# Kernel optimization log

Hardware: AMD Instinct MI355X
Metric: run time of the kernel (lower is better)

Reference implementation:

```python
import jax, jax.numpy as jnp
import numpy as np
import math

B, CZ, L = 1, 128, 256
H, C = 4, 32  # num_heads, head dim
EPS = 1e-5


def _conv1x1(w, x):
    # w: (out, in), x: (b, in, i, j) -> (b, out, i, j)
    return jnp.einsum('oc,bcij->boij', w, x)


def setup_inputs() -> dict:
    key = jax.random.key(0)
    ks = jax.random.split(key, 8)
    s = 1.0 / math.sqrt(CZ)
    return {
        'pair_rep': jax.random.normal(ks[0], (B, CZ, L, L), jnp.float32),
        'ln_gamma': jnp.ones((CZ, L, L), jnp.float32),
        'ln_beta': jnp.zeros((CZ, L, L), jnp.float32),
        'w_q': jax.random.normal(ks[1], (H * C, CZ), jnp.float32) * s,
        'w_k': jax.random.normal(ks[2], (H * C, CZ), jnp.float32) * s,
        'w_v': jax.random.normal(ks[3], (H * C, CZ), jnp.float32) * s,
        'w_b': jax.random.normal(ks[4], (H, CZ), jnp.float32) * s,
        'w_g': jax.random.normal(ks[5], (H * C, CZ), jnp.float32) * s,
        'b_g': jnp.zeros((H * C,), jnp.float32),
        'w_rep': jax.random.normal(ks[6], (CZ, H * C), jnp.float32) * s,
        'b_rep': jnp.zeros((CZ,), jnp.float32),
    }


def reference(pair_rep, ln_gamma, ln_beta, w_q, w_k, w_v, w_b, w_g, b_g, w_rep, b_rep):
    # LayerNorm over (c_z, h, w) jointly, full-shape affine (torch LayerNorm([c_z,h,w]))
    mu = jnp.mean(pair_rep, axis=(1, 2, 3), keepdims=True)
    var = jnp.var(pair_rep, axis=(1, 2, 3), keepdims=True)
    x = (pair_rep - mu) * jax.lax.rsqrt(var + EPS) * ln_gamma[None] + ln_beta[None]

    # 1x1 conv projections; channels packed as (h c): channel = h*C + c
    q = _conv1x1(w_q, x).reshape(B, H, C, L, L)  # bhcij
    k = _conv1x1(w_k, x).reshape(B, H, C, L, L)
    v = _conv1x1(w_v, x).reshape(B, H, C, L, L)
    bias = _conv1x1(w_b, x)                       # (b, h, i, j) -> used as bias[b,h,j,k]
    g = jax.nn.sigmoid(_conv1x1(w_g, x) + b_g[None, :, None, None]).reshape(B, H, C, L, L)

    scale = 1.0 / math.sqrt(C)
    # scores[b,h,i,j,k] = scale * sum_c q[b,h,c,i,j] k[b,h,c,i,k] + bias[b,h,j,k]
    scores = scale * jnp.einsum('bhcij,bhcik->bhijk', q, k) + bias[:, :, None, :, :]
    a = jax.nn.softmax(scores, axis=-1)
    # o[b,h,c,i,j] = sum_k a[b,h,i,j,k] v[b,h,c,i,k]  (same math as the 6D broadcast-sum)
    o = g * jnp.einsum('bhijk,bhcik->bhcij', a, v)

    # output repacks channels as (c h): channel = c*H + h
    o = jnp.transpose(o, (0, 2, 1, 3, 4)).reshape(B, C * H, L, L)
    return _conv1x1(w_rep, o) + b_rep[None, :, None, None]
```

## Files before the change

kernel.cpp:

```cpp
#include <hip/hip_runtime.h>
#include <math.h>

#define L 256
#define CZ 128
#define NH 4
#define HD 32
#define P (L*L)
#define NTOT (CZ*P)
#define EPSV 1e-5f
#define SCALE 0.17677669529663687f

typedef unsigned short u16;
typedef _Float16 f16;
typedef __attribute__((ext_vector_type(8))) _Float16 f16x8;
typedef __attribute__((ext_vector_type(4))) _Float16 f16x4;
typedef __attribute__((ext_vector_type(4))) float    f32x4;

__device__ __forceinline__ float bu2f(u16 u){ return __uint_as_float(((unsigned)u) << 16); }
__device__ __forceinline__ u16 f2bu(float x){
  unsigned u = __float_as_uint(x);
  return (u16)((u + 0x7fffu + ((u >> 16) & 1u)) >> 16);
}

__device__ __forceinline__ float ldr(bool fp32, const void* p, size_t i){
  return fp32 ? ((const float*)p)[i] : bu2f(((const u16*)p)[i]);
}
__device__ __forceinline__ void str(bool fp32, void* p, size_t i, float v){
  if (fp32) ((float*)p)[i] = v; else ((u16*)p)[i] = f2bu(v);
}
template<bool FP32>
__device__ __forceinline__ float ldin(const void* p, size_t i){
  return FP32 ? ((const float*)p)[i] : bu2f(((const u16*)p)[i]);
}
template<bool FP32>
__device__ __forceinline__ void stout(void* p, size_t i, float v){
  if (FP32) ((float*)p)[i] = v; else ((u16*)p)[i] = f2bu(v);
}

__device__ __forceinline__ void glds16(const void* g, void* l){
  __builtin_amdgcn_global_load_lds((const __attribute__((address_space(1))) void*)g,
                                   (__attribute__((address_space(3))) void*)l, 16, 0, 0);
}

#define OFF_WQT   16
#define OFF_WKT   (OFF_WQT+16384)
#define OFF_WVT   (OFF_WKT+16384)
#define OFF_WGT   (OFF_WVT+16384)
#define OFF_WREPT (OFF_WGT+16384)
#define OFF_WBT   (OFF_WREPT+16384)
#define OFF_BGF   (OFF_WBT+512)
#define OFF_BREPF (OFF_BGF+128)
#define OFF_BIAS  (OFF_BREPF+128)
#define OFF_XN    344848
#define OFF_ATTO  (OFF_XN+4194304)
#define WS_NEED   (((size_t)OFF_ATTO + 4194304ull)*4ull)

#define GUARD(ws) if (((((const volatile int*)(ws))[2]) != 0) != FP32) return;
#define RFLAG(ws) (((const volatile int*)(ws))[2] != 0)

__global__ __launch_bounds__(256) void detect_zero(const void* pair, float* ws){
  int b = blockIdx.x, t = threadIdx.x;
  if (b > 0){
    ((float4*)(ws + OFF_BIAS))[(size_t)(b-1)*256 + t] = float4{0.f,0.f,0.f,0.f};
    return;
  }
  const u16* u = (const u16*)pair;
  int big = 0;
  for (int k = t; k < 2048; k += 256){
    float av = fabsf(bu2f(u[k]));
    if (!(av < 1e4f)) big = 1;
  }
  __shared__ int sb[256];
  sb[t] = big; __syncthreads();
  for (int off = 128; off > 0; off >>= 1){
    if (t < off) sb[t] |= sb[t+off];
    __syncthreads();
  }
  if (t == 0){ ((int*)ws)[2] = sb[0]; ws[0] = 0.f; ws[1] = 0.f; }
}

__global__ __launch_bounds__(256) void lnprep(const void* __restrict__ pair,
    const void* wq, const void* wk, const void* wv, const void* wg,
    const void* wrep, const void* wb, const void* bg, const void* brep, float* ws){
  bool fp32 = RFLAG(ws);
  int b = blockIdx.x, t = threadIdx.x;
  if (b < 64){
    int idx = b*256 + t;
    int oc = idx >> 7, cin = idx & 127;
    f16* wf = (f16*)(ws + OFF_WQT);
    wf[0*16384 + idx] = (f16)ldr(fp32, wq, idx);
    wf[1*16384 + idx] = (f16)ldr(fp32, wk, idx);
    wf[2*16384 + idx] = (f16)ldr(fp32, wv, idx);
    wf[3*16384 + idx] = (f16)ldr(fp32, wg, idx);
    float wr = ldr(fp32, wrep, idx);
    ws[OFF_WREPT + cin*128 + oc] = wr;
    ((f16*)(ws + OFF_WVT))[oc*128 + (cin&3)*32 + (cin>>2)] = (f16)wr;
    if (idx < 512){ int h = idx >> 7, ci = idx & 127; ws[OFF_WBT + ci*4 + h] = ldr(fp32, wb, idx); }
    if (idx < 128){ ws[OFF_BGF + idx] = ldr(fp32, bg, idx); ws[OFF_BREPF + idx] = ldr(fp32, brep, idx); }
  }
  int g = b*256 + t;
  float s = 0.f, ss = 0.f;
  if (fp32){
    #pragma unroll
    for (int u = 0; u < 4; ++u){
      float4 v = ((const float4*)pair)[(size_t)u*524288 + g];
      s += v.x+v.y+v.z+v.w;
      ss += v.x*v.x + v.y*v.y + v.z*v.z + v.w*v.w;
    }
  } else {
    #pragma unroll
    for (int u = 0; u < 4; ++u){
      ushort4 v = ((const ushort4*)pair)[(size_t)u*524288 + g];
      float a = bu2f(v.x), bq = bu2f(v.y), c = bu2f(v.z), d = bu2f(v.w);
      s += a+bq+c+d; ss += a*a+bq*bq+c*c+d*d;
    }
  }
  __shared__ float sa[256], sbf[256];
  sa[t] = s; sbf[t] = ss;
  __syncthreads();
  for (int off = 128; off > 0; off >>= 1){
    if (t < off){ sa[t] += sa[t+off]; sbf[t] += sbf[t+off]; }
    __syncthreads();
  }
  if (t == 0){ atomicAdd(&ws[0], sa[0]); atomicAdd(&ws[1], sbf[0]); }
}


__global__ __launch_bounds__(256) void xnorm(const void* __restrict__ pair,
    const void* __restrict__ gamma, const void* __restrict__ beta, float* __restrict__ ws){
  bool fp32 = RFLAG(ws);
  int a = blockIdx.x & 255, q = blockIdx.x >> 8;
  int t = threadIdx.x;
  int cq = t >> 6, b64 = t & 63, j4 = b64 << 2;
  float mu   = ws[0] * (1.0f/NTOT);
  float var  = ws[1] * (1.0f/NTOT) - mu*mu;
  float rstd = rsqrtf(var + EPSV);
  f16 hv[4][8];
  float pb[4][4];
  #pragma unroll
  for (int col = 0; col < 4; ++col)
    #pragma unroll
    for (int h = 0; h < 4; ++h) pb[col][h] = 0.f;
  #pragma unroll
  for (int ce = 0; ce < 8; ++ce){
    int c = q*32 + cq*8 + ce;
    size_t vi = (size_t)c*16384 + (size_t)a*64 + b64;
    float p0,p1,p2,p3, g0,g1,g2,g3, e0,e1,e2,e3;
    if (fp32){
      float4 pv = ((const float4*)pair)[vi];
      float4 gv = ((const float4*)gamma)[vi];
      float4 bv = ((const float4*)beta)[vi];
      p0=pv.x;p1=pv.y;p2=pv.z;p3=pv.w; g0=gv.x;g1=gv.y;g2=gv.z;g3=gv.w; e0=bv.x;e1=bv.y;e2=bv.z;e3=bv.w;
    } else {
      ushort4 pv = ((const ushort4*)pair)[vi];
      ushort4 gv = ((const ushort4*)gamma)[vi];
      ushort4 bv = ((const ushort4*)beta)[vi];
      p0=bu2f(pv.x);p1=bu2f(pv.y);p2=bu2f(pv.z);p3=bu2f(pv.w);
      g0=bu2f(gv.x);g1=bu2f(gv.y);g2=bu2f(gv.z);g3=bu2f(gv.w);
      e0=bu2f(bv.x);e1=bu2f(bv.y);e2=bu2f(bv.z);e3=bu2f(bv.w);
    }
    float x0 = (p0-mu)*rstd*g0 + e0;
    float x1 = (p1-mu)*rstd*g1 + e1;
    float x2 = (p2-mu)*rstd*g2 + e2;
    float x3 = (p3-mu)*rstd*g3 + e3;
    hv[0][ce] = (f16)x0; hv[1][ce] = (f16)x1; hv[2][ce] = (f16)x2; hv[3][ce] = (f16)x3;
    float4 w4 = *(const float4*)(ws + OFF_WBT + c*4);
    pb[0][0] = fmaf(w4.x, x0, pb[0][0]); pb[0][1] = fmaf(w4.y, x0, pb[0][1]);
    pb[0][2] = fmaf(w4.z, x0, pb[0][2]); pb[0][3] = fmaf(w4.w, x0, pb[0][3]);
    pb[1][0] = fmaf(w4.x, x1, pb[1][0]); pb[1][1] = fmaf(w4.y, x1, pb[1][1]);
    pb[1][2] = fmaf(w4.z, x1, pb[1][2]); pb[1][3] = fmaf(w4.w, x1, pb[1][3]);
    pb[2][0] = fmaf(w4.x, x2, pb[2][0]); pb[2][1] = fmaf(w4.y, x2, pb[2][1]);
    pb[2][2] = fmaf(w4.z, x2, pb[2][2]); pb[2][3] = fmaf(w4.w, x2, pb[2][3]);
    pb[3][0] = fmaf(w4.x, x3, pb[3][0]); pb[3][1] = fmaf(w4.y, x3, pb[3][1]);
    pb[3][2] = fmaf(w4.z, x3, pb[3][2]); pb[3][3] = fmaf(w4.w, x3, pb[3][3]);
  }
  char* xnb = (char*)ws + (size_t)OFF_XN*4;
  int cb = q*4 + cq;
  #pragma unroll
  for (int col = 0; col < 4; ++col){
    f16x8 v;
    #pragma unroll
    for (int ce = 0; ce < 8; ++ce) v[ce] = hv[col][ce];
    *(f16x8*)(xnb + ((((size_t)a*16 + cb)*256) + (j4+col))*16) = v;
  }
  __shared__ float sbb[4][64][16];
  #pragma unroll
  for (int col = 0; col < 4; ++col)
    #pragma unroll
    for (int h = 0; h < 4; ++h) sbb[cq][b64][h*4+col] = pb[col][h];
  __syncthreads();
  #pragma unroll
  for (int k = 0; k < 4; ++k){
    int lin = k*256 + t;
    int bb = lin >> 4, hc = lin & 15;
    float v = sbb[0][bb][hc] + sbb[1][bb][hc] + sbb[2][bb][hc] + sbb[3][bb][hc];
    int h = hc >> 2, col = hc & 3;
    atomicAdd(&ws[OFF_BIAS + h*P + a*256 + bb*4 + col], v - 1.0f);
  }
}

__global__ __launch_bounds__(256, 4) void attn_xn(float* __restrict__ ws){
  __shared__ __align__(16) char smem[32768];
  char* Ab = smem;
  char* Bb = smem + 16384;
  const int t = threadIdx.x;
  int bid = blockIdx.x;
  int W = (bid & 7)*128 + (bid >> 3);
  const int i = W >> 2, h = W & 3;
  const int w = t >> 6, l = t & 63;
  const int l15 = l & 15, l4 = l >> 4;
  const char* xnb = (const char*)ws + (size_t)OFF_XN*4 + (size_t)i*65536;
  const f16* wf = (const f16*)(ws + OFF_WQT);

  auto stage = [&](int q){
    #pragma unroll
    for (int cbl = 0; cbl < 4; ++cbl){
      int jsrc = (w*64 + l) ^ cbl;
      const char* src = xnb + (size_t)((q*4 + cbl)*4096) + (size_t)jsrc*16;
      glds16(src, Ab + cbl*4096 + w*1024);
    }
  };

  f32x4 acc[2][4][2];
  auto projpass = [&](int pr0){
    #pragma unroll
    for (int pp = 0; pp < 2; ++pp)
      #pragma unroll
      for (int mj = 0; mj < 4; ++mj)
        #pragma unroll
        for (int nt = 0; nt < 2; ++nt) acc[pp][mj][nt] = f32x4{0.f,0.f,0.f,0.f};
    #pragma unroll
    for (int q = 0; q < 4; ++q){
      __syncthreads();
      f16x8 A[4];
      #pragma unroll
      for (int mj = 0; mj < 4; ++mj){
        int j = 64*w + 16*mj + l15;
        A[mj] = *(const f16x8*)(Ab + l4*4096 + ((j ^ l4)*16));
      }
      __syncthreads();
      if (q < 3) stage(q+1);
      #pragma unroll
      for (int pp = 0; pp < 2; ++pp){
        #pragma unroll
        for (int nt = 0; nt < 2; ++nt){
          int o = h*32 + nt*16 + l15;
          f16x8 Bf = *(const f16x8*)(wf + (pr0+pp)*16384 + o*128 + q*32 + 8*l4);
          #pragma unroll
          for (int mj = 0; mj < 4; ++mj)
            acc[pp][mj][nt] = __builtin_amdgcn_mfma_f32_16x16x32_f16(A[mj], Bf, acc[pp][mj][nt], 0, 0, 0);
        }
      }
    }
  };

  stage(0);
  projpass(0);
  __syncthreads();
  stage(0);
  #pragma unroll
  for (int mj = 0; mj < 4; ++mj){
    #pragma unroll
    for (int nt = 0; nt < 2; ++nt){
      int ob = 2*nt + (l15 >> 3), oe = l15 & 7;
      int kb4 = 64*w + 16*mj + 4*l4;
      #pragma unroll
      for (int r = 0; r < 4; ++r)
        *(f16*)(Bb + ((ob*4096 + (kb4+r)*16 + oe*2) ^ ((ob&3)<<4))) = (f16)acc[0][mj][nt][r];
    }
  }
  __syncthreads();
  f16x8 qa[4];
  #pragma unroll
  for (int mj = 0; mj < 4; ++mj){
    int j = 64*w + 16*mj + l15;
    qa[mj] = *(const f16x8*)(Bb + ((l4*4096 + j*16) ^ ((l4&3)<<4)));
  }
  __syncthreads();
  #pragma unroll
  for (int mj = 0; mj < 4; ++mj){
    #pragma unroll
    for (int nt = 0; nt < 2; ++nt){
      int ob = 2*nt + (l15 >> 3), oe = l15 & 7;
      int kb4 = 64*w + 16*mj + 4*l4;
      #pragma unroll
      for (int r = 0; r < 4; ++r)
        *(f16*)(Bb + ((ob*4096 + (kb4+r)*16 + oe*2) ^ ((ob&3)<<4))) = (f16)acc[1][mj][nt][r];
    }
  }

  projpass(2);
  f16x4 gsh[4][2];
  #pragma unroll
  for (int mj = 0; mj < 4; ++mj){
    #pragma unroll
    for (int nt = 0; nt < 2; ++nt){
      float bgv = ws[OFF_BGF + h*32 + nt*16 + l15];
      #pragma unroll
      for (int r = 0; r < 4; ++r){
        float z = acc[1][mj][nt][r] + bgv;
        gsh[mj][nt][r] = (f16)(1.0f/(1.0f + __expf(-z)));
      }
    }
  }
  __syncthreads();
  #pragma unroll
  for (int mj = 0; mj < 4; ++mj){
    #pragma unroll
    for (int nt = 0; nt < 2; ++nt){
      int c = nt*16 + l15;
      int kkq = 16*w + 4*mj + l4;
      f16x4 pv;
      #pragma unroll
      for (int r = 0; r < 4; ++r) pv[r] = (f16)acc[0][mj][nt][r];
      *(f16x4*)(Ab + kkq*256 + ((c*8) ^ (l4<<3))) = pv;
    }
  }
  __syncthreads();

  f32x4 oacc[4][2];
  #pragma unroll
  for (int mj = 0; mj < 4; ++mj)
    #pragma unroll
    for (int nt = 0; nt < 2; ++nt) oacc[mj][nt] = f32x4{0.f,0.f,0.f,0.f};
  float lp[4] = {0.f,0.f,0.f,0.f};
  const float* bias2 = ws + OFF_BIAS + (size_t)h*P;
  const f32x4 zz = {0.f,0.f,0.f,0.f};

  for (int kt = 0; kt < 8; ++kt){
    int kk0 = kt*32, kkq0 = kt*8;
    float4 bvv[4][2];
    #pragma unroll
    for (int mj = 0; mj < 4; ++mj){
      const float* bp = bias2 + (size_t)(64*w + 16*mj + l15)*256 + kk0 + 4*l4;
      bvv[mj][0] = *(const float4*)bp;
      bvv[mj][1] = *(const float4*)(bp + 16);
    }
    f16x8 kbf[2];
    #pragma unroll
    for (int tt = 0; tt < 2; ++tt)
      kbf[tt] = *(const f16x8*)(Bb + ((l4*4096 + (kk0+16*tt+l15)*16) ^ ((l4&3)<<4)));
    f16x4 vb[2][2];
    #pragma unroll
    for (int tt = 0; tt < 2; ++tt)
      #pragma unroll
      for (int nt = 0; nt < 2; ++nt)
        vb[tt][nt] = *(const f16x4*)(Ab + (kkq0+4*tt+l4)*256 + ((((l15+16*nt)*8)) ^ (l4<<3)));
    #pragma unroll
    for (int mj = 0; mj < 4; ++mj){
      #pragma unroll
      for (int tt = 0; tt < 2; ++tt){
        f32x4 s = __builtin_amdgcn_mfma_f32_16x16x32_f16(kbf[tt], qa[mj], zz, 0, 0, 0);
        float4 bv = bvv[mj][tt];
        f16x4 pa;
        {
          float e0 = __expf(fmaf(s[0], SCALE, bv.x));
          float e1 = __expf(fmaf(s[1], SCALE, bv.y));
          float e2 = __expf(fmaf(s[2], SCALE, bv.z));
          float e3 = __expf(fmaf(s[3], SCALE, bv.w));
          lp[mj] += (e0+e1)+(e2+e3);
          pa[0]=(f16)e0; pa[1]=(f16)e1; pa[2]=(f16)e2; pa[3]=(f16)e3;
        }
        #pragma unroll
        for (int nt = 0; nt < 2; ++nt)
          oacc[mj][nt] = __builtin_amdgcn_mfma_f32_16x16x16f16(pa, vb[tt][nt], oacc[mj][nt], 0, 0, 0);
      }
    }
  }

  float inv[4];
  #pragma unroll
  for (int mj = 0; mj < 4; ++mj){
    float v = lp[mj];
    v += __shfl_xor(v, 16);
    v += __shfl_xor(v, 32);
    inv[mj] = 1.0f / v;
  }
  __syncthreads();
  #pragma unroll
  for (int mj = 0; mj < 4; ++mj){
    #pragma unroll
    for (int r = 0; r < 4; ++r){
      float iv = __shfl(inv[mj], 20*l4 + r);
      int j = 64*w + 16*mj + 4*l4 + r;
      int swz = ((j>>2)&3)<<4;
      #pragma unroll
      for (int nt = 0; nt < 2; ++nt){
        int c = nt*16 + l15;
        float ov = oacc[mj][nt][r] * iv * (float)gsh[mj][nt][r];
        *(f16*)(Bb + ((j*64 + c*2) ^ swz)) = (f16)ov;
      }
    }
  }
  __syncthreads();
  char* ao = (char*)ws + (size_t)OFF_ATTO*4 + (size_t)h*4194304 + ((size_t)i*256)*64;
  #pragma unroll
  for (int u = 0; u < 4; ++u){
    int lin = u*256 + t;
    int j = lin >> 2;
    f16x8 v = *(const f16x8*)(Bb + ((j*64 + (lin&3)*16) ^ (((j>>2)&3)<<4)));
    *(f16x8*)(ao + (size_t)lin*16) = v;
  }
}

__global__ __launch_bounds__(256, 4) void out_proj_mf(float* __restrict__ ws, void* __restrict__ outp){
  bool fp32 = RFLAG(ws);
  __shared__ __align__(16) char smem[32768];
  char* Ab = smem;
  char* Ob = smem + 16384;
  const int t = threadIdx.x;
  int bid = blockIdx.x;
  int W = (bid & 7)*128 + (bid >> 3);
  const int i = W >> 2, oh = W & 3;
  const int w = t >> 6, l = t & 63;
  const int l15 = l & 15, l4 = l >> 4;
  const char* aob = (const char*)ws + (size_t)OFF_ATTO*4;
  const f16* w2 = (const f16*)(ws + OFF_WVT);

  auto stage = [&](int q){
    #pragma unroll
    for (int cbl = 0; cbl < 4; ++cbl){
      int jsrc = (w*64 + l) ^ cbl;
      const char* src = aob + (size_t)q*4194304 + ((size_t)i*256 + jsrc)*64 + cbl*16;
      glds16(src, Ab + cbl*4096 + w*1024);
    }
  };

  f32x4 acc[2][4];
  #pragma unroll
  for (int nt = 0; nt < 2; ++nt)
    #pragma unroll
    for (int mj = 0; mj < 4; ++mj) acc[nt][mj] = f32x4{0.f,0.f,0.f,0.f};

  stage(0);
  #pragma unroll
  for (int q = 0; q < 4; ++q){
    __syncthreads();
    f16x8 A[4];
    #pragma unroll
    for (int mj = 0; mj < 4; ++mj){
      int j = 64*w + 16*mj + l15;
      A[mj] = *(const f16x8*)(Ab + l4*4096 + ((j ^ l4)*16));
    }
    __syncthreads();
    if (q < 3) stage(q+1);
    #pragma unroll
    for (int nt = 0; nt < 2; ++nt){
      int oc = oh*32 + nt*16 + l15;
      f16x8 Bf = *(const f16x8*)(w2 + oc*128 + q*32 + 8*l4);
      #pragma unroll
      for (int mj = 0; mj < 4; ++mj)
        acc[nt][mj] = __builtin_amdgcn_mfma_f32_16x16x32_f16(A[mj], Bf, acc[nt][mj], 0, 0, 0);
    }
  }
  #pragma unroll
  for (int nt = 0; nt < 2; ++nt){
    __syncthreads();
    #pragma unroll
    for (int mj = 0; mj < 4; ++mj){
      #pragma unroll
      for (int r = 0; r < 4; ++r){
        int j = 64*w + 16*mj + 4*l4 + r;
        *(float*)(Ob + l15*1024 + ((j*4) ^ ((l15&7)<<4))) = acc[nt][mj][r];
      }
    }
    __syncthreads();
    #pragma unroll
    for (int o2 = 0; o2 < 16; ++o2){
      int oc = oh*32 + nt*16 + o2;
      float v = *(const float*)(Ob + o2*1024 + ((t*4) ^ ((o2&7)<<4)));
      str(fp32, outp, (size_t)oc*P + (size_t)i*L + t, v + ws[OFF_BREPF + oc]);
    }
  }
}


template<bool FP32>
__global__ __launch_bounds__(256) void bias_old(const void* __restrict__ pair,
    const void* __restrict__ gamma, const void* __restrict__ beta, float* __restrict__ ws){
  GUARD(ws);
  int a = blockIdx.x & 255, q = blockIdx.x >> 8, b = threadIdx.x;
  float mu   = ws[0] * (1.0f/NTOT);
  float var  = ws[1] * (1.0f/NTOT) - mu*mu;
  float rstd = rsqrtf(var + EPSV);
  float a0=0.f, a1=0.f, a2=0.f, a3=0.f;
  int c0 = q*32;
  for (int cc = 0; cc < 32; ++cc){
    int c = c0 + cc;
    size_t idx = (size_t)c*P + (size_t)a*L + b;
    float xv = (ldin<FP32>(pair,idx) - mu)*rstd*ldin<FP32>(gamma,idx) + ldin<FP32>(beta,idx);
    const float* w4 = ws + OFF_WBT + c*4;
    a0 = fmaf(w4[0], xv, a0); a1 = fmaf(w4[1], xv, a1);
    a2 = fmaf(w4[2], xv, a2); a3 = fmaf(w4[3], xv, a3);
  }
  atomicAdd(&ws[OFF_BIAS + 0*P + a*L + b], a0);
  atomicAdd(&ws[OFF_BIAS + 1*P + a*L + b], a1);
  atomicAdd(&ws[OFF_BIAS + 2*P + a*L + b], a2);
  atomicAdd(&ws[OFF_BIAS + 3*P + a*L + b], a3);
}

template<bool FP32>
__global__ __launch_bounds__(256, 2) void attn_old(const void* __restrict__ pair,
    const void* __restrict__ gamma, const void* __restrict__ beta,
    float* __restrict__ ws, void* __restrict__ outp){
  GUARD(ws);
  __shared__ __align__(16) char smem[65536];
  char* Ab  = smem;
  char* KTb = smem + 32768;
  char* V2b = smem + 49152;
  const int t = threadIdx.x;
  const int h = blockIdx.x >> 8, i = blockIdx.x & 255;
  const int w = t >> 6, l = t & 63;
  const int l15 = l & 15, l4 = l >> 4;
  const float mu   = ws[0] * (1.0f/NTOT);
  const float var  = ws[1] * (1.0f/NTOT) - mu*mu;
  const float rstd = rsqrtf(var + EPSV);
  const f16* wf = (const f16*)(ws + OFF_WQT);
  f32x4 acc[4][4][2];
  #pragma unroll
  for (int pr=0;pr<4;++pr)
    #pragma unroll
    for(int mj=0;mj<4;++mj)
      #pragma unroll
      for(int nt=0;nt<2;++nt) acc[pr][mj][nt] = f32x4{0.f,0.f,0.f,0.f};
  for (int half = 0; half < 2; ++half){
    #pragma unroll
    for (int cb = 0; cb < 8; ++cb){
      int cc0 = cb*8;
      f16x8 hv;
      #pragma unroll
      for (int e = 0; e < 8; ++e){
        size_t idx = (size_t)(half*64 + cc0 + e)*P + (size_t)i*L + t;
        float xv = (ldin<FP32>(pair,idx) - mu)*rstd*ldin<FP32>(gamma,idx) + ldin<FP32>(beta,idx);
        hv[e] = (f16)xv;
      }
      *(f16x8*)(Ab + t*128 + ((cc0*2) ^ ((t&7)<<4))) = hv;
    }
    __syncthreads();
    #pragma unroll
    for (int ksl = 0; ksl < 2; ++ksl){
      int cin0 = half*64 + ksl*32;
      f16x8 A[4];
      #pragma unroll
      for (int mj = 0; mj < 4; ++mj){
        int j = 64*w + 16*mj + l15;
        A[mj] = *(const f16x8*)(Ab + j*128 + (((ksl*32 + 8*l4)*2) ^ ((j&7)<<4)));
      }
      #pragma unroll
      for (int pr = 0; pr < 4; ++pr){
        #pragma unroll
        for (int nt = 0; nt < 2; ++nt){
          int o = h*32 + nt*16 + l15;
          f16x8 Bf = *(const f16x8*)(wf + pr*16384 + o*128 + cin0 + 8*l4);
          #pragma unroll
          for (int mj = 0; mj < 4; ++mj)
            acc[pr][mj][nt] = __builtin_amdgcn_mfma_f32_16x16x32_f16(A[mj], Bf, acc[pr][mj][nt], 0, 0, 0);
        }
      }
    }
    __syncthreads();
  }
  f32x4 gs[4][2];
  #pragma unroll
  for (int mj = 0; mj < 4; ++mj){
    #pragma unroll
    for (int nt = 0; nt < 2; ++nt){
      float bgv = ws[OFF_BGF + h*32 + nt*16 + l15];
      #pragma unroll
      for (int r = 0; r < 4; ++r){
        float z = acc[3][mj][nt][r] + bgv;
        gs[mj][nt][r] = 1.0f/(1.0f + __expf(-z));
      }
    }
  }
  #pragma unroll
  for (int mj = 0; mj < 4; ++mj){
    #pragma unroll
    for (int nt = 0; nt < 2; ++nt){
      int o = nt*16 + l15;
      int kb4 = 64*w + 16*mj + 4*l4;
      f16x4 pv;
      #pragma unroll
      for (int r = 0; r < 4; ++r){
        int j = kb4 + r;
        *(f16*)(Ab  + j*64 + ((o*2) ^ ((j&3)<<4))) = (f16)acc[0][mj][nt][r];
        *(f16*)(KTb + j*64 + ((o*2) ^ ((j&3)<<4))) = (f16)acc[1][mj][nt][r];
        pv[r] = (f16)acc[2][mj][nt][r];
      }
      *(f16x4*)(V2b + o*512 + ((kb4*2) ^ ((o&7)<<4))) = pv;
    }
  }
  __syncthreads();
  f16x8 qa[4];
  #pragma unroll
  for (int mj = 0; mj < 4; ++mj){
    int j = 64*w + 16*mj + l15;
    qa[mj] = *(const f16x8*)(Ab + j*64 + ((16*l4) ^ ((j&3)<<4)));
  }
  __syncthreads();
  f32x4 oacc[4][2];
  #pragma unroll
  for (int mj=0;mj<4;++mj)
    #pragma unroll
    for(int nt=0;nt<2;++nt) oacc[mj][nt] = f32x4{0.f,0.f,0.f,0.f};
  float lp[16];
  #pragma unroll
  for (int u = 0; u < 16; ++u) lp[u] = 0.f;
  const float* bias2 = ws + OFF_BIAS + (size_t)h*P;
  const f32x4 zz = {0.f,0.f,0.f,0.f};
  for (int kt = 0; kt < 4; ++kt){
    int kk0 = kt*64;
    #pragma unroll
    for (int nk = 0; nk < 4; ++nk){
      int kkr = kk0 + nk*16 + l15;
      f16x8 kbf = *(const f16x8*)(KTb + kkr*64 + ((16*l4) ^ ((kkr&3)<<4)));
      #pragma unroll
      for (int mj = 0; mj < 4; ++mj){
        f32x4 s = __builtin_amdgcn_mfma_f32_16x16x32_f16(qa[mj], kbf, zz, 0, 0, 0);
        #pragma unroll
        for (int r = 0; r < 4; ++r){
          int j = 64*w + 16*mj + 4*l4 + r;
          float bv = bias2[(size_t)j*L + kkr] - 4.0f;
          float e = __expf(fmaf(s[r], SCALE, bv));
          lp[mj*4+r] += e;
          *(f16*)(Ab + j*128 + (((nk*16+l15)*2) ^ ((j&7)<<4))) = (f16)e;
        }
      }
    }
    __syncthreads();
    #pragma unroll
    for (int ks2 = 0; ks2 < 2; ++ks2){
      f16x8 vb[2];
      #pragma unroll
      for (int nt = 0; nt < 2; ++nt){
        int c = nt*16 + l15;
        vb[nt] = *(const f16x8*)(V2b + c*512 + (((kk0 + ks2*32 + 8*l4)*2) ^ ((c&7)<<4)));
      }
      #pragma unroll
      for (int mj = 0; mj < 4; ++mj){
        int j = 64*w + 16*mj + l15;
        f16x8 pa = *(const f16x8*)(Ab + j*128 + (((ks2*32 + 8*l4)*2) ^ ((j&7)<<4)));
        #pragma unroll
        for (int nt = 0; nt < 2; ++nt)
          oacc[mj][nt] = __builtin_amdgcn_mfma_f32_16x16x32_f16(pa, vb[nt], oacc[mj][nt], 0, 0, 0);
      }
    }
  }
  __syncthreads();
  #pragma unroll
  for (int u = 0; u < 16; ++u){
    float v = lp[u];
    v += __shfl_xor(v, 1);
    v += __shfl_xor(v, 2);
    v += __shfl_xor(v, 4);
    v += __shfl_xor(v, 8);
    lp[u] = 1.0f / v;
  }
  #pragma unroll
  for (int mj = 0; mj < 4; ++mj){
    #pragma unroll
    for (int nt = 0; nt < 2; ++nt){
      int c = nt*16 + l15;
      #pragma unroll
      for (int r = 0; r < 4; ++r){
        int j = 64*w + 16*mj + 4*l4 + r;
        float ov = oacc[mj][nt][r] * lp[mj*4+r] * gs[mj][nt][r];
        *(float*)(Ab + c*1024 + ((j*4) ^ ((c&7)<<4))) = ov;
      }
    }
  }
  __syncthreads();
  #pragma unroll
  for (int c = 0; c < 32; ++c){
    float v = *(const float*)(Ab + c*1024 + ((t*4) ^ ((c&7)<<4)));
    stout<FP32>(outp, (size_t)(c*NH + h)*P + (size_t)i*L + t, v);
  }
}

template<bool FP32>
__global__ __launch_bounds__(256) void out_proj_old(float* __restrict__ ws, void* __restrict__ outp){
  GUARD(ws);
  __shared__ float gos[CZ*65];
  int blk = blockIdx.x;
  int i = blk >> 2, jb = (blk & 3) << 6;
  int t = threadIdx.x;
  for (int u = 0; u < 32; ++u){
    int lin = u*256 + t;
    int m = lin >> 6, p = lin & 63;
    gos[m*65 + p] = ldin<FP32>(outp, (size_t)m*P + (size_t)i*L + jb + p);
  }
  __syncthreads();
  int p = t & 63, w4 = t >> 6;
  int woc = w4*32;
  float acc[32];
  #pragma unroll
  for (int o = 0; o < 32; ++o) acc[o] = 0.f;
  for (int cin = 0; cin < CZ; ++cin){
    float xv = gos[cin*65 + p];
    const float* wrow = ws + OFF_WREPT + cin*128 + woc;
    #pragma unroll
    for (int o = 0; o < 32; ++o) acc[o] = fmaf(wrow[o], xv, acc[o]);
  }
  #pragma unroll
  for (int o = 0; o < 32; ++o){
    int oc = woc + o;
    stout<FP32>(outp, (size_t)oc*P + (size_t)i*L + jb + p, acc[o] + ws[OFF_BREPF + oc]);
  }
}

extern "C" void kernel_launch(void* const* d_in, const int* in_sizes, int n_in,
                              void* d_out, int out_size, void* d_ws, size_t ws_size,
                              hipStream_t stream) {
  (void)in_sizes; (void)n_in; (void)out_size;
  const void* pair  = d_in[0];
  const void* gamma = d_in[1];
  const void* beta  = d_in[2];
  const void* wq    = d_in[3];
  const void* wk    = d_in[4];
  const void* wv    = d_in[5];
  const void* wb    = d_in[6];
  const void* wg    = d_in[7];
  const void* bg    = d_in[8];
  const void* wrep  = d_in[9];
  const void* brep  = d_in[10];
  float* ws = (float*)d_ws;
  bool big = ws_size >= WS_NEED;

  detect_zero<<<257,  256, 0, stream>>>(pair, ws);
  lnprep     <<<2048, 256, 0, stream>>>(pair, wq, wk, wv, wg, wrep, wb, bg, brep, ws);

  if (big){
    xnorm      <<<1024, 256, 0, stream>>>(pair, gamma, beta, ws);
    attn_xn    <<<1024, 256, 0, stream>>>(ws);
    out_proj_mf<<<1024, 256, 0, stream>>>(ws, d_out);
  } else {
    bias_old<false>    <<<1024, 256, 0, stream>>>(pair, gamma, beta, ws);
    bias_old<true>     <<<1024, 256, 0, stream>>>(pair, gamma, beta, ws);
    attn_old<false>    <<<1024, 256, 0, stream>>>(pair, gamma, beta, ws, d_out);
    attn_old<true>     <<<1024, 256, 0, stream>>>(pair, gamma, beta, ws, d_out);
    out_proj_old<false><<<1024, 256, 0, stream>>>(ws, d_out);
    out_proj_old<true> <<<1024, 256, 0, stream>>>(ws, d_out);
  }
}
```

Baseline: 302.5 us.

## Use nontemporal loads/stores, fold log2e into bias for exp2, unroll key loop

Replaces plain global loads and stores in the stats, normalisation, attention-output and output-projection kernels with nontemporal variants to reduce cache pollution on streaming data. Pre-scales the pair bias by log2(e) and scales the score factor so softmax uses exp2f, which drops a multiply per exponential. Fully unrolls the 8-iteration key-tile loop in the attention kernel. Nontemporal hints may hurt when later kernels reread the same buffers (the normalised activations and attention output are consumed soon after), and the unroll raises register pressure.

```diff
diff --git a/kernel.cpp b/kernel.cpp
--- a/kernel.cpp
+++ b/kernel.cpp
@@ -9,12 +9,16 @@
 #define NTOT (CZ*P)
 #define EPSV 1e-5f
 #define SCALE 0.17677669529663687f
+#define LOG2E 1.4426950408889634f
+#define SC2   (SCALE*LOG2E)
 
 typedef unsigned short u16;
 typedef _Float16 f16;
 typedef __attribute__((ext_vector_type(8))) _Float16 f16x8;
 typedef __attribute__((ext_vector_type(4))) _Float16 f16x4;
 typedef __attribute__((ext_vector_type(4))) float    f32x4;
+typedef __attribute__((ext_vector_type(4))) float    fv4;
+typedef __attribute__((ext_vector_type(4))) unsigned short usv4;
 
 __device__ __forceinline__ float bu2f(u16 u){ return __uint_as_float(((unsigned)u) << 16); }
 __device__ __forceinline__ u16 f2bu(float x){
@@ -27,6 +31,10 @@
 }
 __device__ __forceinline__ void str(bool fp32, void* p, size_t i, float v){
   if (fp32) ((float*)p)[i] = v; else ((u16*)p)[i] = f2bu(v);
+}
+__device__ __forceinline__ void strnt(bool fp32, void* p, size_t i, float v){
+  if (fp32) __builtin_nontemporal_store(v, (float*)p + i);
+  else      __builtin_nontemporal_store(f2bu(v), (u16*)p + i);
 }
 template<bool FP32>
 __device__ __forceinline__ float ldin(const void* p, size_t i){
@@ -103,15 +111,15 @@
   if (fp32){
     #pragma unroll
     for (int u = 0; u < 4; ++u){
-      float4 v = ((const float4*)pair)[(size_t)u*524288 + g];
-      s += v.x+v.y+v.z+v.w;
-      ss += v.x*v.x + v.y*v.y + v.z*v.z + v.w*v.w;
+      fv4 v = __builtin_nontemporal_load((const fv4*)pair + (size_t)u*524288 + g);
+      s += v[0]+v[1]+v[2]+v[3];
+      ss += v[0]*v[0] + v[1]*v[1] + v[2]*v[2] + v[3]*v[3];
     }
   } else {
     #pragma unroll
     for (int u = 0; u < 4; ++u){
-      ushort4 v = ((const ushort4*)pair)[(size_t)u*524288 + g];
-      float a = bu2f(v.x), bq = bu2f(v.y), c = bu2f(v.z), d = bu2f(v.w);
+      usv4 v = __builtin_nontemporal_load((const usv4*)pair + (size_t)u*524288 + g);
+      float a = bu2f(v[0]), bq = bu2f(v[1]), c = bu2f(v[2]), d = bu2f(v[3]);
       s += a+bq+c+d; ss += a*a+bq*bq+c*c+d*d;
     }
   }
@@ -147,17 +155,18 @@
     size_t vi = (size_t)c*16384 + (size_t)a*64 + b64;
     float p0,p1,p2,p3, g0,g1,g2,g3, e0,e1,e2,e3;
     if (fp32){
-      float4 pv = ((const float4*)pair)[vi];
-      float4 gv = ((const float4*)gamma)[vi];
-      float4 bv = ((const float4*)beta)[vi];
-      p0=pv.x;p1=pv.y;p2=pv.z;p3=pv.w; g0=gv.x;g1=gv.y;g2=gv.z;g3=gv.w; e0=bv.x;e1=bv.y;e2=bv.z;e3=bv.w;
+      fv4 pv = __builtin_nontemporal_load((const fv4*)pair + vi);
+      fv4 gv = __builtin_nontemporal_load((const fv4*)gamma + vi);
+      fv4 bv = __builtin_nontemporal_load((const fv4*)beta + vi);
+      p0=pv[0];p1=pv[1];p2=pv[2];p3=pv[3]; g0=gv[0];g1=gv[1];g2=gv[2];g3=gv[3];
+      e0=bv[0];e1=bv[1];e2=bv[2];e3=bv[3];
     } else {
-      ushort4 pv = ((const ushort4*)pair)[vi];
-      ushort4 gv = ((const ushort4*)gamma)[vi];
-      ushort4 bv = ((const ushort4*)beta)[vi];
-      p0=bu2f(pv.x);p1=bu2f(pv.y);p2=bu2f(pv.z);p3=bu2f(pv.w);
-      g0=bu2f(gv.x);g1=bu2f(gv.y);g2=bu2f(gv.z);g3=bu2f(gv.w);
-      e0=bu2f(bv.x);e1=bu2f(bv.y);e2=bu2f(bv.z);e3=bu2f(bv.w);
+      usv4 pv = __builtin_nontemporal_load((const usv4*)pair + vi);
+      usv4 gv = __builtin_nontemporal_load((const usv4*)gamma + vi);
+      usv4 bv = __builtin_nontemporal_load((const usv4*)beta + vi);
+      p0=bu2f(pv[0]);p1=bu2f(pv[1]);p2=bu2f(pv[2]);p3=bu2f(pv[3]);
+      g0=bu2f(gv[0]);g1=bu2f(gv[1]);g2=bu2f(gv[2]);g3=bu2f(gv[3]);
+      e0=bu2f(bv[0]);e1=bu2f(bv[1]);e2=bu2f(bv[2]);e3=bu2f(bv[3]);
     }
     float x0 = (p0-mu)*rstd*g0 + e0;
     float x1 = (p1-mu)*rstd*g1 + e1;
@@ -181,7 +190,7 @@
     f16x8 v;
     #pragma unroll
     for (int ce = 0; ce < 8; ++ce) v[ce] = hv[col][ce];
-    *(f16x8*)(xnb + ((((size_t)a*16 + cb)*256) + (j4+col))*16) = v;
+    __builtin_nontemporal_store(v, (f16x8*)(xnb + ((((size_t)a*16 + cb)*256) + (j4+col))*16));
   }
   __shared__ float sbb[4][64][16];
   #pragma unroll
@@ -195,7 +204,7 @@
     int bb = lin >> 4, hc = lin & 15;
     float v = sbb[0][bb][hc] + sbb[1][bb][hc] + sbb[2][bb][hc] + sbb[3][bb][hc];
     int h = hc >> 2, col = hc & 3;
-    atomicAdd(&ws[OFF_BIAS + h*P + a*256 + bb*4 + col], v - 1.0f);
+    atomicAdd(&ws[OFF_BIAS + h*P + a*256 + bb*4 + col], fmaf(v, LOG2E, -LOG2E));
   }
 }
 
@@ -327,6 +336,7 @@
   const float* bias2 = ws + OFF_BIAS + (size_t)h*P;
   const f32x4 zz = {0.f,0.f,0.f,0.f};
 
+  #pragma unroll
   for (int kt = 0; kt < 8; ++kt){
     int kk0 = kt*32, kkq0 = kt*8;
     float4 bvv[4][2];
@@ -354,10 +364,10 @@
         float4 bv = bvv[mj][tt];
         f16x4 pa;
         {
-          float e0 = __expf(fmaf(s[0], SCALE, bv.x));
-          float e1 = __expf(fmaf(s[1], SCALE, bv.y));
-          float e2 = __expf(fmaf(s[2], SCALE, bv.z));
-          float e3 = __expf(fmaf(s[3], SCALE, bv.w));
+          float e0 = exp2f(fmaf(s[0], SC2, bv.x));
+          float e1 = exp2f(fmaf(s[1], SC2, bv.y));
+          float e2 = exp2f(fmaf(s[2], SC2, bv.z));
+          float e3 = exp2f(fmaf(s[3], SC2, bv.w));
           lp[mj] += (e0+e1)+(e2+e3);
           pa[0]=(f16)e0; pa[1]=(f16)e1; pa[2]=(f16)e2; pa[3]=(f16)e3;
         }
@@ -399,7 +409,7 @@
     int lin = u*256 + t;
     int j = lin >> 2;
     f16x8 v = *(const f16x8*)(Bb + ((j*64 + (lin&3)*16) ^ (((j>>2)&3)<<4)));
-    *(f16x8*)(ao + (size_t)lin*16) = v;
+    __builtin_nontemporal_store(v, (f16x8*)(ao + (size_t)lin*16));
   }
 }
 
@@ -469,7 +479,7 @@
     for (int o2 = 0; o2 < 16; ++o2){
       int oc = oh*32 + nt*16 + o2;
       float v = *(const float*)(Ob + o2*1024 + ((t*4) ^ ((o2&7)<<4)));
-      str(fp32, outp, (size_t)oc*P + (size_t)i*L + t, v + ws[OFF_BREPF + oc]);
+      strnt(fp32, outp, (size_t)oc*P + (size_t)i*L + t, v + ws[OFF_BREPF + oc]);
     }
   }
 }
```

Result: slower. 320.4 us (+5.9%).
